# Kernel optimization log

Measured on AMD Instinct MI355X. Metric: run time of the kernel, lower is better.

## Reference

```python
import jax, jax.numpy as jnp
import numpy as np

D_MODEL = 1024

def setup_inputs() -> dict:
    key = jax.random.key(0)
    ks = jax.random.split(key, 9)
    D = D_MODEL
    s = 1.0 / np.sqrt(D)
    return {
        "X": jax.random.normal(ks[0], (4, 2048, D), dtype=jnp.float32),
        "Wq": jax.random.uniform(ks[1], (D, D), jnp.float32, -s, s),
        "bq": jax.random.uniform(ks[2], (D,), jnp.float32, -s, s),
        "Wk": jax.random.uniform(ks[3], (D, D), jnp.float32, -s, s),
        "bk": jax.random.uniform(ks[4], (D,), jnp.float32, -s, s),
        "Wv": jax.random.uniform(ks[5], (D, D), jnp.float32, -s, s),
        "bv": jax.random.uniform(ks[6], (D,), jnp.float32, -s, s),
        "Wo": jax.random.uniform(ks[7], (D, D), jnp.float32, -s, s),
        "bo": jax.random.uniform(ks[8], (D,), jnp.float32, -s, s),
    }

def reference(X, Wq, bq, Wk, bk, Wv, bv, Wo, bo):
    B, N, D = X.shape
    # torch nn.Linear: x @ W.T + b
    q = jnp.einsum('bnd,ed->bne', X, Wq) + bq
    k = jnp.einsum('bnd,ed->bne', X, Wk) + bk
    v = jnp.einsum('bnd,ed->bne', X, Wv) + bv
    scores = jnp.einsum('bqd,bkd->bqk', q, k) / jnp.sqrt(jnp.float32(D))
    # faithful to source: tril ones kept as +1.0, zeros -> -inf, added to scores
    tril = jnp.tril(jnp.ones((N, N), dtype=bool))
    mask = jnp.where(tril, jnp.float32(1.0), jnp.float32(-jnp.inf))
    scores = scores + mask
    weights = jax.nn.softmax(scores, axis=-1)
    ctx = jnp.einsum('bqk,bkd->bqd', weights, v)
    return jnp.einsum('bnd,ed->bne', ctx, Wo) + bo
```

## Files before the change

kernel.cpp:

```cpp
#include <hip/hip_runtime.h>
#include <hip/hip_bf16.h>
#include <stdint.h>


typedef __hip_bfloat16 bf16;
typedef short bf16x8v __attribute__((ext_vector_type(8)));
typedef short bf16x4v __attribute__((ext_vector_type(4)));
typedef float f32x4   __attribute__((ext_vector_type(4)));

#define DEV static __device__ __forceinline__

DEV void gload_lds16(const void* g, void* l) {
  __builtin_amdgcn_global_load_lds(
      (const __attribute__((address_space(1))) void*)g,
      (__attribute__((address_space(3))) void*)l, 16u, 0, 0u);
}

struct alignas(8) bf16q { bf16 a, b, c, d; };

__global__ __launch_bounds__(256)
void k_f32_to_bf16(const float* __restrict__ in, bf16* __restrict__ out, long n4) {
  long i = (long)blockIdx.x * blockDim.x + threadIdx.x;
  if (i >= n4) return;
  float4 v = ((const float4*)in)[i];
  bf16q o{__float2bfloat16(v.x), __float2bfloat16(v.y),
          __float2bfloat16(v.z), __float2bfloat16(v.w)};
  ((bf16q*)out)[i] = o;
}

template<bool OUT_BF16, bool HAS_BIAS, int CAUSAL>
__global__ __launch_bounds__(256)
void k_gemm_bt(const bf16* __restrict__ A, const bf16* __restrict__ B,
               const float* __restrict__ bias, void* __restrict__ Cout,
               int M, int N, int K, float scale,
               long sA, long sB, long sC)
{
  const int tn = blockIdx.x, tm = blockIdx.y, bz = blockIdx.z;
  if (CAUSAL == 1 && tn > tm) return;
  const bf16* Ab = A + (long)bz * sA;
  const bf16* Bb = B + (long)bz * sB;

  __shared__ bf16 As[128 * 32];
  __shared__ bf16 Bs[128 * 32];

  const int t = threadIdx.x;
  const int lane = t & 63;
  const int w = t >> 6;
  const int wr = w >> 1, wc = w & 1;

  f32x4 acc[4][4] = {};

  const int m0 = tm * 128, n0 = tn * 128;
  const int srow = t >> 2;
  const int scol = (t & 3) * 8;

  int kend = K;
  if (CAUSAL == 2) { int ke = (tm + 1) * 128; kend = ke < K ? ke : K; }

  const int fr = lane & 15;
  const int kc = (lane >> 4) * 8;

  for (int k0 = 0; k0 < kend; k0 += 32) {
#pragma unroll
    for (int r = 0; r < 2; ++r) {
      int row = srow + r * 64;
      gload_lds16(Ab + (long)(m0 + row) * K + (k0 + scol), &As[row * 32 + scol]);
      gload_lds16(Bb + (long)(n0 + row) * K + (k0 + scol), &Bs[row * 32 + scol]);
    }
    __syncthreads();

    bf16x8v af[4], bf_[4];
#pragma unroll
    for (int i = 0; i < 4; i++)
      af[i] = *(const bf16x8v*)&As[(wr * 64 + i * 16 + fr) * 32 + kc];
#pragma unroll
    for (int j = 0; j < 4; j++)
      bf_[j] = *(const bf16x8v*)&Bs[(wc * 64 + j * 16 + fr) * 32 + kc];

#pragma unroll
    for (int i = 0; i < 4; i++)
#pragma unroll
      for (int j = 0; j < 4; j++)
        acc[i][j] = __builtin_amdgcn_mfma_f32_16x16x32_bf16(af[i], bf_[j], acc[i][j], 0, 0, 0);

    __syncthreads();
  }

  const int rq = (lane >> 4) * 4;
#pragma unroll
  for (int i = 0; i < 4; i++) {
#pragma unroll
    for (int j = 0; j < 4; j++) {
#pragma unroll
      for (int r = 0; r < 4; r++) {
        int m = m0 + wr * 64 + i * 16 + rq + r;
        int n = n0 + wc * 64 + j * 16 + fr;
        float v = acc[i][j][r] * scale;
        if (HAS_BIAS) v += bias[n];
        if (OUT_BF16)
          ((bf16*)Cout + (long)bz * sC)[(long)m * N + n] = __float2bfloat16(v);
        else
          ((float*)Cout + (long)bz * sC)[(long)m * N + n] = v;
      }
    }
  }
}

__global__ __launch_bounds__(256)
void k_softmax_causal(const float* __restrict__ S, bf16* __restrict__ P) {
  const long row = blockIdx.x;
  const int q = (int)(row & 2047);
  const float* s = S + row * 2048;
  bf16* p = P + row * 2048;
  const int t = threadIdx.x;

  float e[8];
  float m = -3.4e38f;
#pragma unroll
  for (int i = 0; i < 8; i++) {
    int k = t + i * 256;
    float v = (k <= q) ? s[k] : -3.4e38f;
    e[i] = v;
    m = fmaxf(m, v);
  }
#pragma unroll
  for (int off = 1; off < 64; off <<= 1) m = fmaxf(m, __shfl_xor(m, off, 64));
  __shared__ float red[8];
  if ((t & 63) == 0) red[t >> 6] = m;
  __syncthreads();
  m = fmaxf(fmaxf(red[0], red[1]), fmaxf(red[2], red[3]));

  float sum = 0.f;
#pragma unroll
  for (int i = 0; i < 8; i++) {
    int k = t + i * 256;
    float x = (k <= q) ? __expf(e[i] - m) : 0.f;
    e[i] = x;
    sum += x;
  }
#pragma unroll
  for (int off = 1; off < 64; off <<= 1) sum += __shfl_xor(sum, off, 64);
  if ((t & 63) == 0) red[4 + (t >> 6)] = sum;
  __syncthreads();
  sum = red[4] + red[5] + red[6] + red[7];
  float inv = 1.f / sum;
#pragma unroll
  for (int i = 0; i < 8; i++) {
    int k = t + i * 256;
    p[k] = __float2bfloat16(e[i] * inv);
  }
}

__global__ __launch_bounds__(256)
void k_transpose_bf16(const bf16* __restrict__ V, bf16* __restrict__ Vt,
                      int rows, int cols) {
  __shared__ bf16 tile[64][68];
  const long bo = (long)blockIdx.z * (long)rows * cols;
  const bf16* v = V + bo;
  bf16* vt = Vt + bo;
  const int k0 = blockIdx.y * 64;
  const int d0 = blockIdx.x * 64;
  const int t = threadIdx.x;
  const int c4 = (t & 15) * 4;
  const int r = t >> 4;
#pragma unroll
  for (int p2 = 0; p2 < 4; p2++) {
    int row = r + p2 * 16;
    bf16x4v val = *(const bf16x4v*)&v[(long)(k0 + row) * cols + d0 + c4];
    *(bf16x4v*)&tile[row][c4] = val;
  }
  __syncthreads();
#pragma unroll
  for (int p2 = 0; p2 < 4; p2++) {
    int drow = r + p2 * 16;
    bf16q o{tile[c4 + 0][drow], tile[c4 + 1][drow],
            tile[c4 + 2][drow], tile[c4 + 3][drow]};
    *(bf16q*)&vt[(long)(d0 + drow) * rows + k0 + c4] = o;
  }
}

extern "C" void kernel_launch(void* const* d_in, const int* in_sizes, int n_in,
                              void* d_out, int out_size, void* d_ws, size_t ws_size,
                              hipStream_t stream)
{
  const float* X  = (const float*)d_in[0];
  const float* Wq = (const float*)d_in[1];
  const float* bq = (const float*)d_in[2];
  const float* Wk = (const float*)d_in[3];
  const float* bk = (const float*)d_in[4];
  const float* Wv = (const float*)d_in[5];
  const float* bv = (const float*)d_in[6];
  const float* Wo = (const float*)d_in[7];
  const float* bo = (const float*)d_in[8];

  const long Nt = 2048, D = 1024;
  const long TOK = 4 * Nt;

  char* ws = (char*)d_ws;
  const size_t MB = 1024 * 1024;
  bf16* Xb  = (bf16*)(ws + 0);
  bf16* Wqb = (bf16*)(ws + 16 * MB);
  bf16* Wkb = (bf16*)(ws + 18 * MB);
  bf16* Wvb = (bf16*)(ws + 20 * MB);
  bf16* Wob = (bf16*)(ws + 22 * MB);
  bf16* Qb  = (bf16*)(ws + 24 * MB);
  bf16* Kb  = (bf16*)(ws + 40 * MB);
  bf16* Vb  = (bf16*)(ws + 56 * MB);
  bf16* Vt  = (bf16*)(ws + 72 * MB);
  bf16* Cx  = (bf16*)(ws + 88 * MB);
  float* Sf = (float*)(ws + 104 * MB);
  bf16* Pb  = (bf16*)(ws + 168 * MB);

  dim3 blk(256);

  k_f32_to_bf16<<<dim3(8192), blk, 0, stream>>>(X,  Xb,  TOK * D / 4);
  k_f32_to_bf16<<<dim3(1024), blk, 0, stream>>>(Wq, Wqb, D * D / 4);
  k_f32_to_bf16<<<dim3(1024), blk, 0, stream>>>(Wk, Wkb, D * D / 4);
  k_f32_to_bf16<<<dim3(1024), blk, 0, stream>>>(Wv, Wvb, D * D / 4);
  k_f32_to_bf16<<<dim3(1024), blk, 0, stream>>>(Wo, Wob, D * D / 4);

  k_gemm_bt<true, true, 0><<<dim3(8, 64, 1), blk, 0, stream>>>(
      Xb, Wqb, bq, Qb, 8192, 1024, 1024, 1.f, 0, 0, 0);
  k_gemm_bt<true, true, 0><<<dim3(8, 64, 1), blk, 0, stream>>>(
      Xb, Wkb, bk, Kb, 8192, 1024, 1024, 1.f, 0, 0, 0);
  k_gemm_bt<true, true, 0><<<dim3(8, 64, 1), blk, 0, stream>>>(
      Xb, Wvb, bv, Vb, 8192, 1024, 1024, 1.f, 0, 0, 0);

  k_transpose_bf16<<<dim3(16, 32, 4), blk, 0, stream>>>(Vb, Vt, 2048, 1024);

  k_gemm_bt<false, false, 1><<<dim3(16, 16, 4), blk, 0, stream>>>(
      Qb, Kb, nullptr, Sf, 2048, 2048, 1024, 0.03125f,
      Nt * D, Nt * D, Nt * Nt);

  k_softmax_causal<<<dim3(8192), blk, 0, stream>>>(Sf, Pb);

  k_gemm_bt<true, false, 2><<<dim3(8, 16, 4), blk, 0, stream>>>(
      Pb, Vt, nullptr, Cx, 2048, 1024, 2048, 1.f,
      Nt * Nt, D * Nt, Nt * D);

  k_gemm_bt<false, true, 0><<<dim3(8, 64, 1), blk, 0, stream>>>(
      Cx, Wob, bo, d_out, 8192, 1024, 1024, 1.f, 0, 0, 0);
}
```

Baseline: 378.1 us.

## Fuse QKV projections into one GEMM, double-buffer LDS, skip masked softmax writes

Concatenates Wq/Wk/Wv into one bf16 weight matrix and runs a single N=3072 projection GEMM writing an interleaved QKV buffer. Adds lda/ldb/ldc strides so the later kernels read Q, K and V from that buffer. The GEMM now double-buffers its LDS tiles so the next K-slice load overlaps with the MFMA work. The softmax skips writing probabilities beyond the causal block the PV GEMM reads, and the workspace is compacted with the score buffer aliasing the bf16 X copy.

```diff
diff --git a/kernel.cpp b/kernel.cpp
--- a/kernel.cpp
+++ b/kernel.cpp
@@ -33,6 +33,7 @@
 void k_gemm_bt(const bf16* __restrict__ A, const bf16* __restrict__ B,
                const float* __restrict__ bias, void* __restrict__ Cout,
                int M, int N, int K, float scale,
+               int lda, int ldb, int ldc,
                long sA, long sB, long sC)
 {
   const int tn = blockIdx.x, tm = blockIdx.y, bz = blockIdx.z;
@@ -40,8 +41,8 @@
   const bf16* Ab = A + (long)bz * sA;
   const bf16* Bb = B + (long)bz * sB;
 
-  __shared__ bf16 As[128 * 32];
-  __shared__ bf16 Bs[128 * 32];
+  __shared__ bf16 As[2][128 * 32];
+  __shared__ bf16 Bs[2][128 * 32];
 
   const int t = threadIdx.x;
   const int lane = t & 63;
@@ -56,26 +57,38 @@
 
   int kend = K;
   if (CAUSAL == 2) { int ke = (tm + 1) * 128; kend = ke < K ? ke : K; }
+  const int nt = kend >> 5;
 
   const int fr = lane & 15;
   const int kc = (lane >> 4) * 8;
 
-  for (int k0 = 0; k0 < kend; k0 += 32) {
-#pragma unroll
-    for (int r = 0; r < 2; ++r) {
-      int row = srow + r * 64;
-      gload_lds16(Ab + (long)(m0 + row) * K + (k0 + scol), &As[row * 32 + scol]);
-      gload_lds16(Bb + (long)(n0 + row) * K + (k0 + scol), &Bs[row * 32 + scol]);
+#pragma unroll
+  for (int r = 0; r < 2; ++r) {
+    int row = srow + r * 64;
+    gload_lds16(Ab + (long)(m0 + row) * lda + scol, &As[0][row * 32 + scol]);
+    gload_lds16(Bb + (long)(n0 + row) * ldb + scol, &Bs[0][row * 32 + scol]);
+  }
+  __syncthreads();
+
+  int cur = 0;
+  for (int ts = 0; ts < nt; ++ts) {
+    if (ts + 1 < nt) {
+      int k0 = (ts + 1) << 5;
+#pragma unroll
+      for (int r = 0; r < 2; ++r) {
+        int row = srow + r * 64;
+        gload_lds16(Ab + (long)(m0 + row) * lda + (k0 + scol), &As[cur ^ 1][row * 32 + scol]);
+        gload_lds16(Bb + (long)(n0 + row) * ldb + (k0 + scol), &Bs[cur ^ 1][row * 32 + scol]);
+      }
     }
-    __syncthreads();
 
     bf16x8v af[4], bf_[4];
 #pragma unroll
     for (int i = 0; i < 4; i++)
-      af[i] = *(const bf16x8v*)&As[(wr * 64 + i * 16 + fr) * 32 + kc];
+      af[i] = *(const bf16x8v*)&As[cur][(wr * 64 + i * 16 + fr) * 32 + kc];
 #pragma unroll
     for (int j = 0; j < 4; j++)
-      bf_[j] = *(const bf16x8v*)&Bs[(wc * 64 + j * 16 + fr) * 32 + kc];
+      bf_[j] = *(const bf16x8v*)&Bs[cur][(wc * 64 + j * 16 + fr) * 32 + kc];
 
 #pragma unroll
     for (int i = 0; i < 4; i++)
@@ -84,6 +97,7 @@
         acc[i][j] = __builtin_amdgcn_mfma_f32_16x16x32_bf16(af[i], bf_[j], acc[i][j], 0, 0, 0);
 
     __syncthreads();
+    cur ^= 1;
   }
 
   const int rq = (lane >> 4) * 4;
@@ -98,9 +112,9 @@
         float v = acc[i][j][r] * scale;
         if (HAS_BIAS) v += bias[n];
         if (OUT_BF16)
-          ((bf16*)Cout + (long)bz * sC)[(long)m * N + n] = __float2bfloat16(v);
+          ((bf16*)Cout + (long)bz * sC)[(long)m * ldc + n] = __float2bfloat16(v);
         else
-          ((float*)Cout + (long)bz * sC)[(long)m * N + n] = v;
+          ((float*)Cout + (long)bz * sC)[(long)m * ldc + n] = v;
       }
     }
   }
@@ -110,6 +124,7 @@
 void k_softmax_causal(const float* __restrict__ S, bf16* __restrict__ P) {
   const long row = blockIdx.x;
   const int q = (int)(row & 2047);
+  const int kend = ((q >> 7) + 1) << 7;
   const float* s = S + row * 2048;
   bf16* p = P + row * 2048;
   const int t = threadIdx.x;
@@ -119,7 +134,8 @@
 #pragma unroll
   for (int i = 0; i < 8; i++) {
     int k = t + i * 256;
-    float v = (k <= q) ? s[k] : -3.4e38f;
+    float v = -3.4e38f;
+    if (k <= q) v = s[k];
     e[i] = v;
     m = fmaxf(m, v);
   }
@@ -147,17 +163,16 @@
 #pragma unroll
   for (int i = 0; i < 8; i++) {
     int k = t + i * 256;
-    p[k] = __float2bfloat16(e[i] * inv);
+    if (k < kend) p[k] = __float2bfloat16(e[i] * inv);
   }
 }
 
 __global__ __launch_bounds__(256)
 void k_transpose_bf16(const bf16* __restrict__ V, bf16* __restrict__ Vt,
-                      int rows, int cols) {
+                      int in_ld, int out_ld, long in_bs, long out_bs) {
   __shared__ bf16 tile[64][68];
-  const long bo = (long)blockIdx.z * (long)rows * cols;
-  const bf16* v = V + bo;
-  bf16* vt = Vt + bo;
+  const bf16* v = V + (long)blockIdx.z * in_bs;
+  bf16* vt = Vt + (long)blockIdx.z * out_bs;
   const int k0 = blockIdx.y * 64;
   const int d0 = blockIdx.x * 64;
   const int t = threadIdx.x;
@@ -166,7 +181,7 @@
 #pragma unroll
   for (int p2 = 0; p2 < 4; p2++) {
     int row = r + p2 * 16;
-    bf16x4v val = *(const bf16x4v*)&v[(long)(k0 + row) * cols + d0 + c4];
+    bf16x4v val = *(const bf16x4v*)&v[(long)(k0 + row) * in_ld + d0 + c4];
     *(bf16x4v*)&tile[row][c4] = val;
   }
   __syncthreads();
@@ -175,7 +190,7 @@
     int drow = r + p2 * 16;
     bf16q o{tile[c4 + 0][drow], tile[c4 + 1][drow],
             tile[c4 + 2][drow], tile[c4 + 3][drow]};
-    *(bf16q*)&vt[(long)(d0 + drow) * rows + k0 + c4] = o;
+    *(bf16q*)&vt[(long)(d0 + drow) * out_ld + k0 + c4] = o;
   }
 }
 
@@ -198,46 +213,46 @@
 
   char* ws = (char*)d_ws;
   const size_t MB = 1024 * 1024;
-  bf16* Xb  = (bf16*)(ws + 0);
-  bf16* Wqb = (bf16*)(ws + 16 * MB);
-  bf16* Wkb = (bf16*)(ws + 18 * MB);
-  bf16* Wvb = (bf16*)(ws + 20 * MB);
-  bf16* Wob = (bf16*)(ws + 22 * MB);
-  bf16* Qb  = (bf16*)(ws + 24 * MB);
-  bf16* Kb  = (bf16*)(ws + 40 * MB);
-  bf16* Vb  = (bf16*)(ws + 56 * MB);
-  bf16* Vt  = (bf16*)(ws + 72 * MB);
-  bf16* Cx  = (bf16*)(ws + 88 * MB);
-  float* Sf = (float*)(ws + 104 * MB);
-  bf16* Pb  = (bf16*)(ws + 168 * MB);
+  bf16*  QKVb = (bf16*)(ws + 0);
+  bf16*  Wcat = (bf16*)(ws + 48 * MB);
+  bf16*  Wob  = (bf16*)(ws + 54 * MB);
+  float* bcat = (float*)(ws + 56 * MB);
+  bf16*  Vt   = (bf16*)(ws + 57 * MB);
+  bf16*  Cx   = (bf16*)(ws + 73 * MB);
+  bf16*  Pb   = (bf16*)(ws + 89 * MB);
+  bf16*  Xb   = (bf16*)(ws + 121 * MB);
+  float* Sf   = (float*)(ws + 121 * MB);
 
   dim3 blk(256);
 
   k_f32_to_bf16<<<dim3(8192), blk, 0, stream>>>(X,  Xb,  TOK * D / 4);
-  k_f32_to_bf16<<<dim3(1024), blk, 0, stream>>>(Wq, Wqb, D * D / 4);
-  k_f32_to_bf16<<<dim3(1024), blk, 0, stream>>>(Wk, Wkb, D * D / 4);
-  k_f32_to_bf16<<<dim3(1024), blk, 0, stream>>>(Wv, Wvb, D * D / 4);
-  k_f32_to_bf16<<<dim3(1024), blk, 0, stream>>>(Wo, Wob, D * D / 4);
-
-  k_gemm_bt<true, true, 0><<<dim3(8, 64, 1), blk, 0, stream>>>(
-      Xb, Wqb, bq, Qb, 8192, 1024, 1024, 1.f, 0, 0, 0);
-  k_gemm_bt<true, true, 0><<<dim3(8, 64, 1), blk, 0, stream>>>(
-      Xb, Wkb, bk, Kb, 8192, 1024, 1024, 1.f, 0, 0, 0);
-  k_gemm_bt<true, true, 0><<<dim3(8, 64, 1), blk, 0, stream>>>(
-      Xb, Wvb, bv, Vb, 8192, 1024, 1024, 1.f, 0, 0, 0);
-
-  k_transpose_bf16<<<dim3(16, 32, 4), blk, 0, stream>>>(Vb, Vt, 2048, 1024);
+  k_f32_to_bf16<<<dim3(1024), blk, 0, stream>>>(Wq, Wcat,                Wq ? D * D / 4 : 0);
+  k_f32_to_bf16<<<dim3(1024), blk, 0, stream>>>(Wk, Wcat + D * D,        D * D / 4);
+  k_f32_to_bf16<<<dim3(1024), blk, 0, stream>>>(Wv, Wcat + 2 * D * D,    D * D / 4);
+  k_f32_to_bf16<<<dim3(1024), blk, 0, stream>>>(Wo, Wob,                 D * D / 4);
+
+  hipMemcpyAsync(bcat,        bq, D * 4, hipMemcpyDeviceToDevice, stream);
+  hipMemcpyAsync(bcat + D,    bk, D * 4, hipMemcpyDeviceToDevice, stream);
+  hipMemcpyAsync(bcat + 2*D,  bv, D * 4, hipMemcpyDeviceToDevice, stream);
+
+  k_gemm_bt<true, true, 0><<<dim3(24, 64, 1), blk, 0, stream>>>(
+      Xb, Wcat, bcat, QKVb, 8192, 3072, 1024, 1.f,
+      1024, 1024, 3072, 0, 0, 0);
+
+  k_transpose_bf16<<<dim3(16, 32, 4), blk, 0, stream>>>(
+      QKVb + 2048, Vt, 3072, 2048, Nt * 3072, D * Nt);
 
   k_gemm_bt<false, false, 1><<<dim3(16, 16, 4), blk, 0, stream>>>(
-      Qb, Kb, nullptr, Sf, 2048, 2048, 1024, 0.03125f,
-      Nt * D, Nt * D, Nt * Nt);
+      QKVb, QKVb + 1024, nullptr, Sf, 2048, 2048, 1024, 0.03125f,
+      3072, 3072, 2048, Nt * 3072, Nt * 3072, Nt * Nt);
 
   k_softmax_causal<<<dim3(8192), blk, 0, stream>>>(Sf, Pb);
 
   k_gemm_bt<true, false, 2><<<dim3(8, 16, 4), blk, 0, stream>>>(
       Pb, Vt, nullptr, Cx, 2048, 1024, 2048, 1.f,
-      Nt * Nt, D * Nt, Nt * D);
+      2048, 2048, 1024, Nt * Nt, D * Nt, Nt * D);
 
   k_gemm_bt<false, true, 0><<<dim3(8, 64, 1), blk, 0, stream>>>(
-      Cx, Wob, bo, d_out, 8192, 1024, 1024, 1.f, 0, 0, 0);
-}
+      Cx, Wob, bo, d_out, 8192, 1024, 1024, 1.f,
+      1024, 1024, 1024, 0, 0, 0);
+}
```

Result: faster. 332.3 us (-12.1%).
